# Kernel optimization log

Hardware: AMD Instinct MI355X
Metric: run time of the kernel (lower is better)

Reference implementation:

```python
import jax, jax.numpy as jnp
import numpy as np

N = 262144   # flattened seq_len * num_agents
D = 256      # d_model
H = 256      # expert_hidden_dim
E = 4        # num_experts
C = 10       # num_classes
K = 2        # top-k


def setup_inputs() -> dict:
    key = jax.random.key(0)
    ks = jax.random.split(key, 8)
    def w(k, shape, fan_in):
        return jax.random.normal(k, shape, dtype=jnp.float32) / np.sqrt(fan_in).astype(np.float32)
    return {
        "x":   jax.random.normal(ks[0], (N, D), dtype=jnp.float32),
        # gate: Linear(D,D) -> GELU -> Linear(D,E)
        "Wg1": w(ks[1], (D, D), D), "bg1": jnp.zeros((D,), jnp.float32),
        "Wg2": w(ks[2], (D, E), D), "bg2": jnp.zeros((E,), jnp.float32),
        # experts (stacked): Linear(D,H) -> GELU -> Linear(H,C)
        "We1": w(ks[3], (E, D, H), D), "be1": jnp.zeros((E, H), jnp.float32),
        "We2": w(ks[4], (E, H, C), H), "be2": jnp.zeros((E, C), jnp.float32),
        # alpha head: Linear(D,H) -> GELU -> Linear(H,C) -> Softplus
        "Wa1": w(ks[5], (D, H), D), "ba1": jnp.zeros((H,), jnp.float32),
        "Wa2": w(ks[6], (H, C), H), "ba2": jnp.zeros((C,), jnp.float32),
    }


def reference(x, Wg1, bg1, Wg2, bg2, We1, be1, We2, be2, Wa1, ba1, Wa2, ba2):
    gelu = lambda v: jax.nn.gelu(v, approximate=False)  # torch nn.GELU default (erf)

    # --- noisy top-k gating (eval mode: no noise, no dropout) ---
    gate_logits = gelu(x @ Wg1 + bg1) @ Wg2 + bg2                      # [N, E]
    top_vals, top_idx = jax.lax.top_k(gate_logits, K)                  # [N, K]
    rows = jnp.arange(x.shape[0])[:, None]
    gw = jnp.zeros_like(gate_logits).at[rows, top_idx].set(top_vals)   # scatter top-k vals, zeros elsewhere
    gate_weights = jax.nn.softmax(gw, axis=-1)                         # softmax over ALL E slots (zeros included)
    load = gate_weights.sum(axis=0)                                    # [E]

    # --- dense expert ensemble ---
    h = gelu(jnp.einsum('nd,edh->neh', x, We1) + be1)                  # [N, E, H]
    expert_out = jnp.einsum('neh,ehc->nec', h, We2) + be2              # [N, E, C]
    logits = jnp.einsum('nec,ne->nc', expert_out, gate_weights)        # [N, C]

    # --- Dirichlet alpha head ---
    alpha = jax.nn.softplus(gelu(x @ Wa1 + ba1) @ Wa2 + ba2) + 1e-6    # [N, C]

    return logits, alpha, gate_weights, load
```

## Files before the change

kernel.cpp:

```cpp
#include <hip/hip_runtime.h>
#include <hip/hip_bf16.h>


typedef _Float16 f16x8 __attribute__((ext_vector_type(8)));
typedef _Float16 f16x4 __attribute__((ext_vector_type(4)));
typedef float    f32x4 __attribute__((ext_vector_type(4)));

static constexpr int    NTOK      = 262144;
static constexpr size_t ALPHA_OFF = (size_t)NTOK * 10;
static constexpr size_t GW_OFF    = (size_t)2 * NTOK * 10;
static constexpr size_t LOAD_OFF  = GW_OFF + (size_t)NTOK * 4;

static constexpr size_t W1F_OFF   = 0;
static constexpr size_t W2F_OFF   = 786432;
static constexpr size_t CNT_OFF   = 835584;
static constexpr size_t LIST_OFF  = 835648;
static constexpr size_t LPART_OFF = 1884224;

static constexpr float DELTA = 0.02f;

__device__ __forceinline__ float gelu_exact(float v){
  return 0.5f * v * (1.0f + erff(v * 0.7071067811865475f));
}
__device__ __forceinline__ float gelu_fast(float v){
  float t = v * v;
  float p = __builtin_fmaf(0.0713548162726f, t, 1.5957691216057f);
  float z = __expf(v * p);
  float r = __builtin_amdgcn_rcpf(z + 1.0f);
  return v - v * r;
}
__device__ __forceinline__ float softplus_fast(float v){
  float z = __expf(v);
  float l = __logf(1.0f + z);
  return (v > 15.0f) ? v : l;
}
__device__ __forceinline__ f32x4 mfma16(f16x8 a, f16x8 b, f32x4 c){
  return __builtin_amdgcn_mfma_f32_16x16x32_f16(a, b, c, 0, 0, 0);
}
__device__ __forceinline__ f16x8 pk8(float4 a, float4 b){
  union { f16x8 v; unsigned u[4]; } r;
  r.u[0] = __builtin_bit_cast(unsigned, __builtin_amdgcn_cvt_pkrtz(a.x, a.y));
  r.u[1] = __builtin_bit_cast(unsigned, __builtin_amdgcn_cvt_pkrtz(a.z, a.w));
  r.u[2] = __builtin_bit_cast(unsigned, __builtin_amdgcn_cvt_pkrtz(b.x, b.y));
  r.u[3] = __builtin_bit_cast(unsigned, __builtin_amdgcn_cvt_pkrtz(b.z, b.w));
  return r.v;
}
__device__ __forceinline__ f16x4 pk4(float a, float b, float c, float d){
  union { f16x4 v; unsigned u[2]; } r;
  r.u[0] = __builtin_bit_cast(unsigned, __builtin_amdgcn_cvt_pkrtz(a, b));
  r.u[1] = __builtin_bit_cast(unsigned, __builtin_amdgcn_cvt_pkrtz(c, d));
  return r.v;
}

__device__ __forceinline__ void topk4(float v0, float v1, float v2, float v3,
                                      float4& gw, float& gap, int& i1, int& i2){
  float m1 = fmaxf(fmaxf(v0, v1), fmaxf(v2, v3));
  i1 = (v0 == m1) ? 0 : (v1 == m1) ? 1 : (v2 == m1) ? 2 : 3;
  float m2 = 0.f; i2 = -1;
  if (0 != i1){ m2 = v0; i2 = 0; }
  if (1 != i1 && (i2 < 0 || v1 > m2)){ m2 = v1; i2 = 1; }
  if (2 != i1 && (i2 < 0 || v2 > m2)){ m2 = v2; i2 = 2; }
  if (3 != i1 && (i2 < 0 || v3 > m2)){ m2 = v3; i2 = 3; }
  float m3 = -3.0e38f;
  if (0 != i1 && 0 != i2) m3 = fmaxf(m3, v0);
  if (1 != i1 && 1 != i2) m3 = fmaxf(m3, v1);
  if (2 != i1 && 2 != i2) m3 = fmaxf(m3, v2);
  if (3 != i1 && 3 != i2) m3 = fmaxf(m3, v3);
  gap = m2 - m3;
  float mm = fmaxf(m1, 0.0f);
  float s0 = (0 == i1 || 0 == i2) ? v0 : 0.0f;
  float s1 = (1 == i1 || 1 == i2) ? v1 : 0.0f;
  float s2 = (2 == i1 || 2 == i2) ? v2 : 0.0f;
  float s3 = (3 == i1 || 3 == i2) ? v3 : 0.0f;
  float e0 = expf(s0 - mm), e1 = expf(s1 - mm), e2 = expf(s2 - mm), e3 = expf(s3 - mm);
  float inv = 1.0f / (e0 + e1 + e2 + e3);
  gw.x = e0 * inv; gw.y = e1 * inv; gw.z = e2 * inv; gw.w = e3 * inv;
}

__global__ void prep_w1f(const float* __restrict__ We1, const float* __restrict__ Wa1,
                         const float* __restrict__ Wg1, _Float16* __restrict__ W1F){
  int idx = blockIdx.x * 256 + threadIdx.x;
  int e = idx >> 13;
  int r = idx & 8191;
  int kc = r >> 10;
  int entry = r & 1023;
  int ht = entry >> 6, ll = entry & 63;
  int h = ht * 16 + (ll & 15);
  int d0 = kc * 32 + ((ll >> 4) << 3);
  f16x8 o;
  #pragma unroll
  for (int j = 0; j < 8; ++j){
    int d = d0 + j;
    float v;
    if (e < 4)       v = We1[e * 65536 + d * 256 + h];
    else if (e == 4) v = Wa1[d * 256 + h];
    else             v = Wg1[d * 256 + h];
    o[j] = (_Float16)v;
  }
  *(f16x8*)&W1F[(size_t)idx * 8] = o;
}

__global__ void prep_w2f(const float* __restrict__ We2, const float* __restrict__ Wa2,
                         const float* __restrict__ Wg2, _Float16* __restrict__ W2F,
                         unsigned int* __restrict__ cntp){
  if (blockIdx.x == 0 && threadIdx.x == 0) *cntp = 0;
  int idx = blockIdx.x * 256 + threadIdx.x;
  int e = idx >> 9;
  int r = idx & 511;
  int k2 = r >> 6, ll = r & 63;
  int c = ll & 15;
  int h0 = k2 * 32 + ((ll >> 4) << 3);
  f16x8 o;
  #pragma unroll
  for (int j = 0; j < 8; ++j){
    int h = h0 + j;
    float v = 0.0f;
    if (e < 4){ if (c < 10) v = We2[e * 2560 + h * 10 + c]; }
    else if (e == 4){ if (c < 10) v = Wa2[h * 10 + c]; }
    else { if (c < 4) v = Wg2[h * 4 + c]; }
    o[j] = (_Float16)v;
  }
  *(f16x8*)&W2F[(size_t)idx * 8] = o;
}

__device__ __forceinline__ void run_l1(const _Float16* __restrict__ w1s,
                                       const unsigned char* __restrict__ xsb,
                                       int w, int l, int l15, int lq,
                                       f32x4 acc[2][4]){
  #pragma unroll
  for (int kc = 0; kc < 8; ++kc){
    f16x8 af[2], bf[4];
    #pragma unroll
    for (int i = 0; i < 2; ++i)
      af[i] = *(const f16x8*)&w1s[(size_t)kc * 8192 + (w + 8 * i) * 512 + l * 8];
    #pragma unroll
    for (int tt = 0; tt < 4; ++tt){
      int lt = tt * 16 + l15;
      bf[tt] = *(const f16x8*)(xsb + lt * 512 +
                 ((kc * 64 + lq * 16) ^ ((lt & 15) << 4)));
    }
    __builtin_amdgcn_s_setprio(1);
    #pragma unroll
    for (int i = 0; i < 2; ++i)
      #pragma unroll
      for (int tt = 0; tt < 4; ++tt)
        acc[i][tt] = mfma16(af[i], bf[tt], acc[i][tt]);
    __builtin_amdgcn_s_setprio(0);
  }
}

__global__ __launch_bounds__(512, 4) void fused_kernel(
    const float* __restrict__ x,
    const _Float16* __restrict__ W1F, const _Float16* __restrict__ W2F,
    const float* __restrict__ bg1, const float* __restrict__ bg2,
    const float* __restrict__ be1, const float* __restrict__ be2,
    const float* __restrict__ ba1, const float* __restrict__ ba2,
    float* __restrict__ out, unsigned int* __restrict__ list,
    unsigned int* __restrict__ cntp, float* __restrict__ lpart){
  __shared__ __align__(16) unsigned char lds[65600];
  unsigned char* xsb = lds;
  unsigned char* hs0 = lds + 32768;
  unsigned char* hs1 = lds + 49152;
  float*        lsum = (float*)(lds + 65536);

  const int tid = threadIdx.x;
  const int w = tid >> 6, l = tid & 63;
  const int l15 = l & 15, lq = l >> 4;
  const size_t t0 = (size_t)blockIdx.x * 64;
  const int tokL = (w & 3) * 16 + l15;
  const int key  = (tokL & 15) << 4;

  {
    int d = (tid & 31) * 8;
    #pragma unroll
    for (int q = 0; q < 4; ++q){
      int tk = q * 16 + (tid >> 5);
      const float* xp = x + (t0 + tk) * 256 + d;
      float4 f0 = *(const float4*)xp;
      float4 f1 = *(const float4*)(xp + 4);
      *(f16x8*)(xsb + tk * 512 + ((d * 2) ^ ((tk & 15) << 4))) = pk8(f0, f1);
    }
  }
  __syncthreads();

  f32x4 lacc = {0,0,0,0};
  float4 gw4 = {0,0,0,0};

  #pragma unroll 1
  for (int s = 0; s < 6; ++s){
    const int e = (s == 0) ? 5 : (s - 1);
    f32x4 acc[2][4];
    #pragma unroll
    for (int i = 0; i < 2; ++i)
      #pragma unroll
      for (int tt = 0; tt < 4; ++tt){
        acc[i][tt][0]=0.f; acc[i][tt][1]=0.f; acc[i][tt][2]=0.f; acc[i][tt][3]=0.f;
      }
    run_l1(W1F + (size_t)e * 65536, xsb, w, l, l15, lq, acc);

    const float* b1p = (e == 5) ? bg1 : (e < 4 ? be1 + e * 256 : ba1);
    f32x4 d2 = {0,0,0,0};
    #pragma unroll
    for (int p = 0; p < 2; ++p){
      unsigned char* hb_ = p ? hs1 : hs0;
      {
        int hb = (w + 8 * p) * 16 + lq * 4;
        float4 b4 = *(const float4*)&b1p[hb];
        int lb = (w * 16 + lq * 4) * 2;
        #pragma unroll
        for (int tt = 0; tt < 4; ++tt){
          f16x4 hv = pk4(gelu_fast(acc[p][tt][0] + b4.x),
                         gelu_fast(acc[p][tt][1] + b4.y),
                         gelu_fast(acc[p][tt][2] + b4.z),
                         gelu_fast(acc[p][tt][3] + b4.w));
          int lt = tt * 16 + l15;
          *(f16x4*)(hb_ + lt * 256 + (lb ^ ((lt & 15) << 4))) = hv;
        }
      }
      __syncthreads();
      if (w < 4){
        #pragma unroll
        for (int k2h = 0; k2h < 4; ++k2h){
          int k2 = 4 * p + k2h;
          f16x8 a2 = *(const f16x8*)&W2F[((size_t)(e * 8 + k2) * 64 + l) * 8];
          f16x8 b2 = *(const f16x8*)(hb_ + tokL * 256 + ((k2h * 64 + lq * 16) ^ key));
          d2 = mfma16(a2, b2, d2);
        }
      }
    }

    if (s == 0){
      float4 gw = {0,0,0,0};
      float4 lgw = {0,0,0,0};
      int i1 = 0, i2 = 0;
      bool flagged = false;
      if (lq == 0 && w < 4){
        float v0 = d2[0] + bg2[0], v1 = d2[1] + bg2[1];
        float v2 = d2[2] + bg2[2], v3 = d2[3] + bg2[3];
        float gap;
        topk4(v0, v1, v2, v3, gw, gap, i1, i2);
        size_t t = t0 + tokL;
        *(float4*)&out[GW_OFF + t * 4] = gw;
        flagged = (gap < DELTA);
        lgw = gw;
      }
      gw4.x = __shfl(gw.x, l15, 64);
      gw4.y = __shfl(gw.y, l15, 64);
      gw4.z = __shfl(gw.z, l15, 64);
      gw4.w = __shfl(gw.w, l15, 64);
      if (w < 4){
        unsigned long long m = __ballot(flagged);
        int cnt = __popcll(m);
        if (cnt){
          unsigned base = 0;
          if (l == 0) base = atomicAdd(cntp, (unsigned)cnt);
          base = __shfl(base, 0, 64);
          if (flagged){
            unsigned rank = (unsigned)__popcll(m & ((1ull << l) - 1ull));
            list[base + rank] = (unsigned)(t0 + tokL) | (i1 << 18) | (i2 << 20);
          }
        }
        #pragma unroll
        for (int mm = 1; mm < 64; mm <<= 1){
          lgw.x += __shfl_xor(lgw.x, mm, 64); lgw.y += __shfl_xor(lgw.y, mm, 64);
          lgw.z += __shfl_xor(lgw.z, mm, 64); lgw.w += __shfl_xor(lgw.w, mm, 64);
        }
        if (l == 0) *(float4*)&lsum[w * 4] = lgw;
      }
      __syncthreads();
      if (tid < 4)
        lpart[(size_t)blockIdx.x * 4 + tid] =
            lsum[tid] + lsum[4 + tid] + lsum[8 + tid] + lsum[12 + tid];
    } else if (e < 4){
      if (w < 4){
        float gwv = (e == 0) ? gw4.x : (e == 1) ? gw4.y : (e == 2) ? gw4.z : gw4.w;
        #pragma unroll
        for (int r = 0; r < 4; ++r){
          int c = lq * 4 + r;
          float bv = (c < 10) ? be2[e * 10 + c] : 0.0f;
          lacc[r] += gwv * (d2[r] + bv);
        }
      }
    } else {
      if (w < 4){
        size_t t = t0 + tokL;
        #pragma unroll
        for (int r = 0; r < 4; ++r){
          int c = lq * 4 + r;
          if (c < 10)
            out[ALPHA_OFF + t * 10 + c] = softplus_fast(d2[r] + ba2[c]) + 1e-6f;
        }
      }
    }
  }
  if (w < 4){
    size_t t = t0 + tokL;
    #pragma unroll
    for (int r = 0; r < 4; ++r){
      int c = lq * 4 + r;
      if (c < 10) out[t * 10 + c] = lacc[r];
    }
  }
}

__global__ __launch_bounds__(256) void refine_kernel(
    const float* __restrict__ x, const float* __restrict__ Wg1,
    const float* __restrict__ bg1, const float* __restrict__ Wg2,
    const float* __restrict__ bg2,
    const float* __restrict__ We1, const float* __restrict__ be1,
    const float* __restrict__ We2, const float* __restrict__ be2,
    const unsigned int* __restrict__ list, const unsigned int* __restrict__ cntp,
    float* __restrict__ out){
  int cnt = (int)*cntp;
  int l = threadIdx.x & 63;
  int hb = l * 4;
  for (int idx = blockIdx.x * 4 + (threadIdx.x >> 6); idx < cnt;
       idx += gridDim.x * 4){
    unsigned ent = list[idx];
    int t = (int)(ent & 0x3FFFFu);
    int oi1 = (ent >> 18) & 3, oi2 = (ent >> 20) & 3;
    const float* xr = x + (size_t)t * 256;
    float a0 = 0.f, a1 = 0.f, a2 = 0.f, a3 = 0.f;
    #pragma unroll 8
    for (int d = 0; d < 256; ++d){
      float xv = xr[d];
      float4 wv = *(const float4*)&Wg1[d * 256 + hb];
      a0 = fmaf(xv, wv.x, a0); a1 = fmaf(xv, wv.y, a1);
      a2 = fmaf(xv, wv.z, a2); a3 = fmaf(xv, wv.w, a3);
    }
    float4 b4 = *(const float4*)&bg1[hb];
    float g0 = gelu_exact(a0 + b4.x), g1 = gelu_exact(a1 + b4.y);
    float g2 = gelu_exact(a2 + b4.z), g3 = gelu_exact(a3 + b4.w);
    float4 w0 = *(const float4*)&Wg2[(hb + 0) * 4];
    float4 w1 = *(const float4*)&Wg2[(hb + 1) * 4];
    float4 w2 = *(const float4*)&Wg2[(hb + 2) * 4];
    float4 w3 = *(const float4*)&Wg2[(hb + 3) * 4];
    float p0 = g0 * w0.x + g1 * w1.x + g2 * w2.x + g3 * w3.x;
    float p1 = g0 * w0.y + g1 * w1.y + g2 * w2.y + g3 * w3.y;
    float p2 = g0 * w0.z + g1 * w1.z + g2 * w2.z + g3 * w3.z;
    float p3 = g0 * w0.w + g1 * w1.w + g2 * w2.w + g3 * w3.w;
    #pragma unroll
    for (int m = 1; m < 64; m <<= 1){
      p0 += __shfl_xor(p0, m, 64); p1 += __shfl_xor(p1, m, 64);
      p2 += __shfl_xor(p2, m, 64); p3 += __shfl_xor(p3, m, 64);
    }
    float4 gw; float gap; int i1, i2;
    topk4(p0 + bg2[0], p1 + bg2[1], p2 + bg2[2], p3 + bg2[3], gw, gap, i1, i2);
    if (l == 0) *(float4*)&out[GW_OFF + (size_t)t * 4] = gw;
    int oldset = (1 << oi1) | (1 << oi2);
    int newset = (1 << i1) | (1 << i2);
    if (oldset != newset){
      float lg[10];
      #pragma unroll
      for (int c = 0; c < 10; ++c) lg[c] = 0.f;
      for (int e = 0; e < 4; ++e){
        float gwe = (e == 0) ? gw.x : (e == 1) ? gw.y : (e == 2) ? gw.z : gw.w;
        float c0 = 0.f, c1 = 0.f, c2 = 0.f, c3 = 0.f;
        #pragma unroll 8
        for (int d = 0; d < 256; ++d){
          float xv = xr[d];
          float4 wv = *(const float4*)&We1[e * 65536 + d * 256 + hb];
          c0 = fmaf(xv, wv.x, c0); c1 = fmaf(xv, wv.y, c1);
          c2 = fmaf(xv, wv.z, c2); c3 = fmaf(xv, wv.w, c3);
        }
        float4 be = *(const float4*)&be1[e * 256 + hb];
        float h[4];
        h[0] = gelu_exact(c0 + be.x); h[1] = gelu_exact(c1 + be.y);
        h[2] = gelu_exact(c2 + be.z); h[3] = gelu_exact(c3 + be.w);
        #pragma unroll
        for (int r = 0; r < 4; ++r){
          const float* w2p = &We2[e * 2560 + (hb + r) * 10];
          #pragma unroll
          for (int c = 0; c < 10; ++c) lg[c] += gwe * (h[r] * w2p[c]);
        }
      }
      #pragma unroll
      for (int m = 1; m < 64; m <<= 1)
        #pragma unroll
        for (int c = 0; c < 10; ++c) lg[c] += __shfl_xor(lg[c], m, 64);
      if (l == 0){
        #pragma unroll
        for (int c = 0; c < 10; ++c)
          out[(size_t)t * 10 + c] = lg[c] + gw.x * be2[c] + gw.y * be2[10 + c]
                                         + gw.z * be2[20 + c] + gw.w * be2[30 + c];
      }
    }
  }
}

__global__ void reduce_load(const float* __restrict__ lpart, float* __restrict__ out){
  __shared__ float red[4][4];
  int tid = threadIdx.x;
  const float4* lp = (const float4*)lpart;
  float4 v = {0,0,0,0};
  #pragma unroll
  for (int j = 0; j < 16; ++j){
    float4 t = lp[tid + 256 * j];
    v.x += t.x; v.y += t.y; v.z += t.z; v.w += t.w;
  }
  #pragma unroll
  for (int m = 1; m < 64; m <<= 1){
    v.x += __shfl_xor(v.x, m, 64); v.y += __shfl_xor(v.y, m, 64);
    v.z += __shfl_xor(v.z, m, 64); v.w += __shfl_xor(v.w, m, 64);
  }
  if ((tid & 63) == 0){
    red[tid >> 6][0] = v.x; red[tid >> 6][1] = v.y;
    red[tid >> 6][2] = v.z; red[tid >> 6][3] = v.w;
  }
  __syncthreads();
  if (tid < 4)
    out[LOAD_OFF + tid] = red[0][tid] + red[1][tid] + red[2][tid] + red[3][tid];
}

extern "C" void kernel_launch(void* const* d_in, const int* in_sizes, int n_in,
                              void* d_out, int out_size, void* d_ws, size_t ws_size,
                              hipStream_t stream){
  const float* x   = (const float*)d_in[0];
  const float* Wg1 = (const float*)d_in[1];
  const float* bg1 = (const float*)d_in[2];
  const float* Wg2 = (const float*)d_in[3];
  const float* bg2 = (const float*)d_in[4];
  const float* We1 = (const float*)d_in[5];
  const float* be1 = (const float*)d_in[6];
  const float* We2 = (const float*)d_in[7];
  const float* be2 = (const float*)d_in[8];
  const float* Wa1 = (const float*)d_in[9];
  const float* ba1 = (const float*)d_in[10];
  const float* Wa2 = (const float*)d_in[11];
  const float* ba2 = (const float*)d_in[12];
  float* out = (float*)d_out;

  _Float16* W1F       = (_Float16*)((char*)d_ws + W1F_OFF);
  _Float16* W2F       = (_Float16*)((char*)d_ws + W2F_OFF);
  unsigned int* cntp  = (unsigned int*)((char*)d_ws + CNT_OFF);
  unsigned int* list  = (unsigned int*)((char*)d_ws + LIST_OFF);
  float* lpart        = (float*)((char*)d_ws + LPART_OFF);

  hipLaunchKernelGGL(prep_w1f, dim3(192), dim3(256), 0, stream, We1, Wa1, Wg1, W1F);
  hipLaunchKernelGGL(prep_w2f, dim3(12),  dim3(256), 0, stream, We2, Wa2, Wg2, W2F, cntp);
  hipLaunchKernelGGL(fused_kernel, dim3(4096), dim3(512), 0, stream,
                     x, W1F, W2F, bg1, bg2, be1, be2, ba1, ba2,
                     out, list, cntp, lpart);
  hipLaunchKernelGGL(refine_kernel, dim3(1024), dim3(256), 0, stream,
                     x, Wg1, bg1, Wg2, bg2, We1, be1, We2, be2, list, cntp, out);
  hipLaunchKernelGGL(reduce_load, dim3(1), dim3(256), 0, stream, lpart, out);
}
```

Baseline: 538.4 us.

## Compute gate second layer in fp32 with exact GELU and tighten refine threshold

The gate's hidden activations now use exact erf GELU and are multiplied by Wg2 in fp32 with cross-lane and LDS reductions, replacing the fp16 MFMA path for the gate logits. The more accurate logits allow a smaller near-tie threshold (DELTA), so fewer tokens are flagged for the separate refine kernel that recomputes them exactly. The cost is more scalar ALU work and an extra LDS round trip plus barrier in the gate stage. Fewer refine passes are traded against slower gating.

```diff
diff --git a/kernel.cpp b/kernel.cpp
--- a/kernel.cpp
+++ b/kernel.cpp
@@ -17,7 +17,7 @@
 static constexpr size_t LIST_OFF  = 835648;
 static constexpr size_t LPART_OFF = 1884224;
 
-static constexpr float DELTA = 0.02f;
+static constexpr float DELTA = 0.008f;
 
 __device__ __forceinline__ float gelu_exact(float v){
   return 0.5f * v * (1.0f + erff(v * 0.7071067811865475f));
@@ -152,7 +152,8 @@
 __global__ __launch_bounds__(512, 4) void fused_kernel(
     const float* __restrict__ x,
     const _Float16* __restrict__ W1F, const _Float16* __restrict__ W2F,
-    const float* __restrict__ bg1, const float* __restrict__ bg2,
+    const float* __restrict__ bg1, const float* __restrict__ Wg2,
+    const float* __restrict__ bg2,
     const float* __restrict__ be1, const float* __restrict__ be2,
     const float* __restrict__ ba1, const float* __restrict__ ba2,
     float* __restrict__ out, unsigned int* __restrict__ list,
@@ -161,6 +162,7 @@
   unsigned char* xsb = lds;
   unsigned char* hs0 = lds + 32768;
   unsigned char* hs1 = lds + 49152;
+  float*        gred = (float*)(lds + 32768);
   float*        lsum = (float*)(lds + 65536);
 
   const int tid = threadIdx.x;
@@ -186,9 +188,7 @@
   f32x4 lacc = {0,0,0,0};
   float4 gw4 = {0,0,0,0};
 
-  #pragma unroll 1
-  for (int s = 0; s < 6; ++s){
-    const int e = (s == 0) ? 5 : (s - 1);
+  {
     f32x4 acc[2][4];
     #pragma unroll
     for (int i = 0; i < 2; ++i)
@@ -196,9 +196,102 @@
       for (int tt = 0; tt < 4; ++tt){
         acc[i][tt][0]=0.f; acc[i][tt][1]=0.f; acc[i][tt][2]=0.f; acc[i][tt][3]=0.f;
       }
+    run_l1(W1F + (size_t)5 * 65536, xsb, w, l, l15, lq, acc);
+
+    float gp[4][4];
+    #pragma unroll
+    for (int tt = 0; tt < 4; ++tt){ gp[tt][0]=0.f; gp[tt][1]=0.f; gp[tt][2]=0.f; gp[tt][3]=0.f; }
+    #pragma unroll
+    for (int i = 0; i < 2; ++i){
+      int hbase = (w + 8 * i) * 16 + lq * 4;
+      float4 b4 = *(const float4*)&bg1[hbase];
+      float bb[4] = {b4.x, b4.y, b4.z, b4.w};
+      #pragma unroll
+      for (int r = 0; r < 4; ++r){
+        float4 w2 = *(const float4*)&Wg2[(hbase + r) * 4];
+        #pragma unroll
+        for (int tt = 0; tt < 4; ++tt){
+          float g = gelu_exact(acc[i][tt][r] + bb[r]);
+          gp[tt][0] += g * w2.x; gp[tt][1] += g * w2.y;
+          gp[tt][2] += g * w2.z; gp[tt][3] += g * w2.w;
+        }
+      }
+    }
+    #pragma unroll
+    for (int tt = 0; tt < 4; ++tt)
+      #pragma unroll
+      for (int c = 0; c < 4; ++c){
+        gp[tt][c] += __shfl_xor(gp[tt][c], 16, 64);
+        gp[tt][c] += __shfl_xor(gp[tt][c], 32, 64);
+      }
+    if (lq == 0){
+      #pragma unroll
+      for (int tt = 0; tt < 4; ++tt){
+        float4 v; v.x = gp[tt][0]; v.y = gp[tt][1]; v.z = gp[tt][2]; v.w = gp[tt][3];
+        *(float4*)&gred[(w * 64 + tt * 16 + l15) * 4] = v;
+      }
+    }
+    __syncthreads();
+
+    float4 gw = {0,0,0,0};
+    float4 lgw = {0,0,0,0};
+    int i1 = 0, i2 = 0;
+    bool flagged = false;
+    if (lq == 0 && w < 4){
+      float v0 = bg2[0], v1 = bg2[1], v2 = bg2[2], v3 = bg2[3];
+      #pragma unroll
+      for (int ww = 0; ww < 8; ++ww){
+        float4 s = *(const float4*)&gred[(ww * 64 + tokL) * 4];
+        v0 += s.x; v1 += s.y; v2 += s.z; v3 += s.w;
+      }
+      float gap;
+      topk4(v0, v1, v2, v3, gw, gap, i1, i2);
+      size_t t = t0 + tokL;
+      *(float4*)&out[GW_OFF + t * 4] = gw;
+      flagged = (gap < DELTA);
+      lgw = gw;
+    }
+    gw4.x = __shfl(gw.x, l15, 64);
+    gw4.y = __shfl(gw.y, l15, 64);
+    gw4.z = __shfl(gw.z, l15, 64);
+    gw4.w = __shfl(gw.w, l15, 64);
+    if (w < 4){
+      unsigned long long m = __ballot(flagged);
+      int cnt = __popcll(m);
+      if (cnt){
+        unsigned base = 0;
+        if (l == 0) base = atomicAdd(cntp, (unsigned)cnt);
+        base = __shfl(base, 0, 64);
+        if (flagged){
+          unsigned rank = (unsigned)__popcll(m & ((1ull << l) - 1ull));
+          list[base + rank] = (unsigned)(t0 + tokL) | (i1 << 18) | (i2 << 20);
+        }
+      }
+      #pragma unroll
+      for (int mm = 1; mm < 64; mm <<= 1){
+        lgw.x += __shfl_xor(lgw.x, mm, 64); lgw.y += __shfl_xor(lgw.y, mm, 64);
+        lgw.z += __shfl_xor(lgw.z, mm, 64); lgw.w += __shfl_xor(lgw.w, mm, 64);
+      }
+      if (l == 0) *(float4*)&lsum[w * 4] = lgw;
+    }
+    __syncthreads();
+    if (tid < 4)
+      lpart[(size_t)blockIdx.x * 4 + tid] =
+          lsum[tid] + lsum[4 + tid] + lsum[8 + tid] + lsum[12 + tid];
+  }
+
+  #pragma unroll 1
+  for (int e = 0; e < 5; ++e){
+    f32x4 acc[2][4];
+    #pragma unroll
+    for (int i = 0; i < 2; ++i)
+      #pragma unroll
+      for (int tt = 0; tt < 4; ++tt){
+        acc[i][tt][0]=0.f; acc[i][tt][1]=0.f; acc[i][tt][2]=0.f; acc[i][tt][3]=0.f;
+      }
     run_l1(W1F + (size_t)e * 65536, xsb, w, l, l15, lq, acc);
 
-    const float* b1p = (e == 5) ? bg1 : (e < 4 ? be1 + e * 256 : ba1);
+    const float* b1p = (e < 4) ? (be1 + e * 256) : ba1;
     f32x4 d2 = {0,0,0,0};
     #pragma unroll
     for (int p = 0; p < 2; ++p){
@@ -229,49 +322,7 @@
       }
     }
 
-    if (s == 0){
-      float4 gw = {0,0,0,0};
-      float4 lgw = {0,0,0,0};
-      int i1 = 0, i2 = 0;
-      bool flagged = false;
-      if (lq == 0 && w < 4){
-        float v0 = d2[0] + bg2[0], v1 = d2[1] + bg2[1];
-        float v2 = d2[2] + bg2[2], v3 = d2[3] + bg2[3];
-        float gap;
-        topk4(v0, v1, v2, v3, gw, gap, i1, i2);
-        size_t t = t0 + tokL;
-        *(float4*)&out[GW_OFF + t * 4] = gw;
-        flagged = (gap < DELTA);
-        lgw = gw;
-      }
-      gw4.x = __shfl(gw.x, l15, 64);
-      gw4.y = __shfl(gw.y, l15, 64);
-      gw4.z = __shfl(gw.z, l15, 64);
-      gw4.w = __shfl(gw.w, l15, 64);
-      if (w < 4){
-        unsigned long long m = __ballot(flagged);
-        int cnt = __popcll(m);
-        if (cnt){
-          unsigned base = 0;
-          if (l == 0) base = atomicAdd(cntp, (unsigned)cnt);
-          base = __shfl(base, 0, 64);
-          if (flagged){
-            unsigned rank = (unsigned)__popcll(m & ((1ull << l) - 1ull));
-            list[base + rank] = (unsigned)(t0 + tokL) | (i1 << 18) | (i2 << 20);
-          }
-        }
-        #pragma unroll
-        for (int mm = 1; mm < 64; mm <<= 1){
-          lgw.x += __shfl_xor(lgw.x, mm, 64); lgw.y += __shfl_xor(lgw.y, mm, 64);
-          lgw.z += __shfl_xor(lgw.z, mm, 64); lgw.w += __shfl_xor(lgw.w, mm, 64);
-        }
-        if (l == 0) *(float4*)&lsum[w * 4] = lgw;
-      }
-      __syncthreads();
-      if (tid < 4)
-        lpart[(size_t)blockIdx.x * 4 + tid] =
-            lsum[tid] + lsum[4 + tid] + lsum[8 + tid] + lsum[12 + tid];
-    } else if (e < 4){
+    if (e < 4){
       if (w < 4){
         float gwv = (e == 0) ? gw4.x : (e == 1) ? gw4.y : (e == 2) ? gw4.z : gw4.w;
         #pragma unroll
@@ -439,7 +490,7 @@
   hipLaunchKernelGGL(prep_w1f, dim3(192), dim3(256), 0, stream, We1, Wa1, Wg1, W1F);
   hipLaunchKernelGGL(prep_w2f, dim3(12),  dim3(256), 0, stream, We2, Wa2, Wg2, W2F, cntp);
   hipLaunchKernelGGL(fused_kernel, dim3(4096), dim3(512), 0, stream,
-                     x, W1F, W2F, bg1, bg2, be1, be2, ba1, ba2,
+                     x, W1F, W2F, bg1, Wg2, bg2, be1, be2, ba1, ba2,
                      out, list, cntp, lpart);
   hipLaunchKernelGGL(refine_kernel, dim3(1024), dim3(256), 0, stream,
                      x, Wg1, bg1, Wg2, bg2, We1, be1, We2, be2, list, cntp, out);
```

Result: no change. 547.6 us (+1.7%).
